# Performance work log

Measured on AMD Instinct MI355X. Metric: run time of the kernel, lower is better.

The kernel has to match this reference:

```python
import jax, jax.numpy as jnp
import numpy as np

N_HEADS = 64
N_KV_HEADS = 8
HEAD_DIM = 128
HIDDEN = 8192
SEQ = 2048


def setup_inputs() -> dict:
    key = jax.random.key(0)
    k1, k2, k3, k4 = jax.random.split(key, 4)
    scale = 1.0 / np.sqrt(HIDDEN)
    x = jax.random.normal(k1, (1, 1, SEQ, HIDDEN), dtype=jnp.float32)
    wq = jax.random.normal(k2, (HIDDEN, N_HEADS * HEAD_DIM), dtype=jnp.float32) * scale
    wk = jax.random.normal(k3, (HIDDEN, N_KV_HEADS * HEAD_DIM), dtype=jnp.float32) * scale
    wv = jax.random.normal(k4, (HIDDEN, N_KV_HEADS * HEAD_DIM), dtype=jnp.float32) * scale
    return {"x": x, "wq": wq, "wk": wk, "wv": wv}


def reference(x, wq, wk, wv):
    # Fused QKV projection: concat weights along output dim, single matmul.
    qkv_w = jnp.concatenate([wq, wk, wv], axis=-1)  # [H, (64+8+8)*128]
    fused = jnp.einsum('bush,hd->busd', x, qkv_w)    # [1,1,S,10240]
    b, _, s, _ = fused.shape
    q_dim = N_HEADS * HEAD_DIM
    kv_dim = N_KV_HEADS * HEAD_DIM
    q = fused[..., :q_dim]
    k = fused[..., q_dim:q_dim + kv_dim]
    v = fused[..., q_dim + kv_dim:]
    # nlp_create_qkv_heads: [B,1,S,nh*hd] -> [B,nh,S,hd]
    q_heads = q.reshape(b, s, N_HEADS, HEAD_DIM).transpose(0, 2, 1, 3)
    k_heads = k.reshape(b, s, N_KV_HEADS, HEAD_DIM).transpose(0, 2, 1, 3)
    v_heads = v.reshape(b, s, N_KV_HEADS, HEAD_DIM).transpose(0, 2, 1, 3)
    return (q_heads, k_heads, v_heads)
```

## Files before the change

### kernel.cpp

```cpp
#include <hip/hip_runtime.h>
#include <stdint.h>

#define M_DIM 2048
#define K_DIM 8192
#define N_Q   8192
#define N_KV  1024
#define BM    128
#define BN    128
#define BK    32
#define NIT   (K_DIM / BK)

typedef __bf16 bf16x8 __attribute__((ext_vector_type(8)));
typedef __bf16 bf16x2 __attribute__((ext_vector_type(2)));
typedef float  f32x4  __attribute__((ext_vector_type(4)));

__device__ __forceinline__ uint32_t swz(uint32_t r) { return ((r >> 1) ^ (r >> 3)) & 3u; }

__device__ __forceinline__ uint32_t pack_bf16(float lo, float hi) {
    bf16x2 v = { (__bf16)lo, (__bf16)hi };
    return __builtin_bit_cast(uint32_t, v);
}

__global__ __launch_bounds__(256) void qkv_gemm(
    const float* __restrict__ x,
    const float* __restrict__ wq,
    const float* __restrict__ wk,
    const float* __restrict__ wv,
    float* __restrict__ out)
{
    __shared__ __align__(16) uint16_t sA[BM * BK];
    __shared__ __align__(16) uint16_t sB[BN * BK];
    uint32_t* sAu = (uint32_t*)sA;
    uint32_t* sBu = (uint32_t*)sB;

    const uint32_t tid    = threadIdx.x;
    const uint32_t bid    = blockIdx.x;
    const uint32_t mt_blk = bid & 15;
    const uint32_t nt_blk = bid >> 4;
    const uint32_t m0     = mt_blk * BM;

    const size_t QSZ = (size_t)64 * M_DIM * 128;
    const size_t KSZ = (size_t)8  * M_DIM * 128;
    const float* Wsel;
    uint32_t ldW, col0;
    size_t obase;
    if (nt_blk < 64)      { Wsel = wq; ldW = N_Q;  col0 = nt_blk * 128;
                            obase = (size_t)nt_blk * M_DIM * 128; }
    else if (nt_blk < 72) { Wsel = wk; ldW = N_KV; col0 = (nt_blk - 64) * 128;
                            obase = QSZ + (size_t)(nt_blk - 64) * M_DIM * 128; }
    else                  { Wsel = wv; ldW = N_KV; col0 = (nt_blk - 72) * 128;
                            obase = QSZ + KSZ + (size_t)(nt_blk - 72) * M_DIM * 128; }

    const float* agp = x + (size_t)(m0 + (tid >> 3)) * K_DIM + (tid & 7) * 4;
    uint32_t a_wr[4];
    #pragma unroll
    for (int i = 0; i < 4; ++i) {
        uint32_t r = i * 32 + (tid >> 3);
        a_wr[i] = r * 16 + ((((tid >> 1) & 3) ^ swz(r)) * 4) + (tid & 1) * 2;
    }

    const uint32_t bk  = (tid >> 4) * 2;
    const uint32_t bn0 = (tid & 15) * 8;
    const float* bgp = Wsel + (size_t)bk * ldW + col0 + bn0;
    const uint32_t bkc = bk >> 3;
    const uint32_t bkd = (bk & 7) >> 1;

    f32x4 apre[4], bpre[4];
    #pragma unroll
    for (int i = 0; i < 4; ++i) apre[i] = *(const f32x4*)(agp + (size_t)i * 32 * K_DIM);
    bpre[0] = *(const f32x4*)(bgp);
    bpre[1] = *(const f32x4*)(bgp + 4);
    bpre[2] = *(const f32x4*)(bgp + ldW);
    bpre[3] = *(const f32x4*)(bgp + ldW + 4);

    const uint32_t lane = tid & 63;
    const uint32_t wid  = tid >> 6;
    const uint32_t wm   = (wid >> 1) * 64;
    const uint32_t wn   = (wid & 1) * 64;
    const uint32_t l15  = lane & 15;
    const uint32_t quad = lane >> 4;

    f32x4 acc[4][4] = {};

    uint32_t a_off[4], b_off[4];
    #pragma unroll
    for (int t = 0; t < 4; ++t) {
        uint32_t ar = wm + t * 16 + l15;
        a_off[t] = ar * BK + ((quad ^ swz(ar)) * 8);
        uint32_t br = wn + t * 16 + l15;
        b_off[t] = br * BK + ((quad ^ swz(br)) * 8);
    }

    const float* agp_n = agp + BK;
    const float* bgp_n = bgp + (size_t)BK * ldW;

    for (uint32_t kt = 0; kt < NIT; ++kt) {
        __syncthreads();

        #pragma unroll
        for (int i = 0; i < 4; ++i) {
            uint2 w;
            w.x = pack_bf16(apre[i].x, apre[i].y);
            w.y = pack_bf16(apre[i].z, apre[i].w);
            *(uint2*)&sAu[a_wr[i]] = w;
        }
        {
            const float* pk0 = (const float*)&bpre[0];
            const float* pk1 = (const float*)&bpre[2];
            #pragma unroll
            for (int j = 0; j < 8; ++j) {
                uint32_t n = bn0 + j;
                sBu[n * 16 + ((bkc ^ swz(n)) * 4) + bkd] = pack_bf16(pk0[j], pk1[j]);
            }
        }

        if (kt + 1 < NIT) {
            #pragma unroll
            for (int i = 0; i < 4; ++i) apre[i] = *(const f32x4*)(agp_n + (size_t)i * 32 * K_DIM);
            bpre[0] = *(const f32x4*)(bgp_n);
            bpre[1] = *(const f32x4*)(bgp_n + 4);
            bpre[2] = *(const f32x4*)(bgp_n + ldW);
            bpre[3] = *(const f32x4*)(bgp_n + ldW + 4);
            agp_n += BK;
            bgp_n += (size_t)BK * ldW;
        }

        __syncthreads();

        bf16x8 af[4], bf[4];
        #pragma unroll
        for (int t = 0; t < 4; ++t) {
            af[t] = *(const bf16x8*)(sA + a_off[t]);
            bf[t] = *(const bf16x8*)(sB + b_off[t]);
        }
        #pragma unroll
        for (int mt = 0; mt < 4; ++mt)
            #pragma unroll
            for (int nt = 0; nt < 4; ++nt)
                acc[mt][nt] = __builtin_amdgcn_mfma_f32_16x16x32_bf16(
                    af[mt], bf[nt], acc[mt][nt], 0, 0, 0);
    }

    float* op = out + obase + (size_t)m0 * 128;
    #pragma unroll
    for (int mt = 0; mt < 4; ++mt) {
        #pragma unroll
        for (int r = 0; r < 4; ++r) {
            uint32_t row = wm + mt * 16 + quad * 4 + r;
            #pragma unroll
            for (int nt = 0; nt < 4; ++nt) {
                uint32_t col = wn + nt * 16 + l15;
                op[(size_t)row * 128 + col] = acc[mt][nt][r];
            }
        }
    }
}

extern "C" void kernel_launch(void* const* d_in, const int* in_sizes, int n_in,
                              void* d_out, int out_size, void* d_ws, size_t ws_size,
                              hipStream_t stream) {
    const float* x  = (const float*)d_in[0];
    const float* wq = (const float*)d_in[1];
    const float* wk = (const float*)d_in[2];
    const float* wv = (const float*)d_in[3];
    qkv_gemm<<<dim3((M_DIM / BM) * ((N_Q + 2 * N_KV) / BN)), dim3(256), 0, stream>>>(
        x, wq, wk, wv, (float*)d_out);
}
```

Baseline: 1.032 ms.

## Pre-cast inputs to bf16 in workspace and use direct global-to-LDS GEMM

Adds separate kernels that convert x to bf16 and convert plus transpose the concatenated weights into a K-contiguous bf16 workspace. A new GEMM kernel then streams both operands with global_load_lds 16-byte loads straight into swizzled LDS, and remaps block order for cache locality. This removes per-iteration fp32 loads and in-register conversion and transposed scalar LDS stores. In exchange it pays extra memory passes over the inputs and has no double buffering. It falls back to the old kernel when workspace is too small.

```diff
diff --git a/kernel.cpp b/kernel.cpp
--- a/kernel.cpp
+++ b/kernel.cpp
@@ -5,6 +5,7 @@
 #define K_DIM 8192
 #define N_Q   8192
 #define N_KV  1024
+#define N_TOT (N_Q + 2 * N_KV)
 #define BM    128
 #define BN    128
 #define BK    32
@@ -14,7 +15,147 @@
 typedef __bf16 bf16x2 __attribute__((ext_vector_type(2)));
 typedef float  f32x4  __attribute__((ext_vector_type(4)));
 
-__device__ __forceinline__ uint32_t swz(uint32_t r) { return ((r >> 1) ^ (r >> 3)) & 3u; }
+__global__ __launch_bounds__(256) void xcast(const float* __restrict__ x,
+                                             __bf16* __restrict__ xb) {
+    size_t i = ((size_t)blockIdx.x * 256 + threadIdx.x) * 8;
+    f32x4 a = *(const f32x4*)(x + i);
+    f32x4 b = *(const f32x4*)(x + i + 4);
+    bf16x8 o = { (__bf16)a.x, (__bf16)a.y, (__bf16)a.z, (__bf16)a.w,
+                 (__bf16)b.x, (__bf16)b.y, (__bf16)b.z, (__bf16)b.w };
+    *(bf16x8*)(xb + i) = o;
+}
+
+__global__ __launch_bounds__(256) void wcast_t(const float* __restrict__ wq,
+                                               const float* __restrict__ wk,
+                                               const float* __restrict__ wv,
+                                               __bf16* __restrict__ wt) {
+    __shared__ float sT[64 * 65];
+    const uint32_t bid   = blockIdx.x;
+    const uint32_t ktile = bid & 127;
+    const uint32_t ntile = bid >> 7;
+    const float* W; uint32_t ldW, csrc, cdst;
+    if (ntile < 128)      { W = wq; ldW = N_Q;  csrc = ntile * 64;
+                            cdst = csrc; }
+    else if (ntile < 144) { W = wk; ldW = N_KV; csrc = (ntile - 128) * 64;
+                            cdst = N_Q + csrc; }
+    else                  { W = wv; ldW = N_KV; csrc = (ntile - 144) * 64;
+                            cdst = N_Q + N_KV + csrc; }
+    const uint32_t k0 = ktile * 64;
+    const uint32_t t  = threadIdx.x;
+
+    const uint32_t lr = t >> 4;
+    const uint32_t lc = (t & 15) * 4;
+    const float* gp = W + (size_t)(k0 + lr) * ldW + csrc + lc;
+    #pragma unroll
+    for (int i = 0; i < 4; ++i) {
+        f32x4 v = *(const f32x4*)(gp + (size_t)i * 16 * ldW);
+        float* d = &sT[(lr + i * 16) * 65 + lc];
+        d[0] = v.x; d[1] = v.y; d[2] = v.z; d[3] = v.w;
+    }
+    __syncthreads();
+
+    const uint32_t wn  = t >> 3;
+    const uint32_t wk8 = (t & 7) * 8;
+    #pragma unroll
+    for (int it = 0; it < 2; ++it) {
+        uint32_t n = wn + it * 32;
+        bf16x8 o;
+        #pragma unroll
+        for (int j = 0; j < 8; ++j) o[j] = (__bf16)sT[(wk8 + j) * 65 + n];
+        *(bf16x8*)(wt + (size_t)(cdst + n) * K_DIM + k0 + wk8) = o;
+    }
+}
+
+__device__ __forceinline__ void gload16(const void* g, void* l) {
+    __builtin_amdgcn_global_load_lds(
+        (const __attribute__((address_space(1))) void*)g,
+        (__attribute__((address_space(3))) void*)l, 16, 0, 0);
+}
+
+__global__ __launch_bounds__(256) void qkv_mm(const __bf16* __restrict__ xb,
+                                              const __bf16* __restrict__ wt,
+                                              float* __restrict__ out) {
+    __shared__ __align__(16) __bf16 sA[BM * BK];
+    __shared__ __align__(16) __bf16 sB[BN * BK];
+
+    const uint32_t tid = threadIdx.x;
+
+    const uint32_t logical = (blockIdx.x & 7) * 160 + (blockIdx.x >> 3);
+    const uint32_t mt = logical & 15;
+    const uint32_t nt = logical >> 4;
+    const uint32_t m0 = mt * BM;
+    const uint32_t n0 = nt * BN;
+
+    const uint32_t w    = tid >> 6;
+    const uint32_t lane = tid & 63;
+    const __bf16* gA[2];
+    const __bf16* gB[2];
+    #pragma unroll
+    for (int i = 0; i < 2; ++i) {
+        uint32_t c  = w * 128 + i * 64 + lane;
+        uint32_t r  = c >> 2;
+        uint32_t qs = (c & 3) ^ ((r >> 1) & 3);
+        gA[i] = xb + (size_t)(m0 + r) * K_DIM + qs * 8;
+        gB[i] = wt + (size_t)(n0 + r) * K_DIM + qs * 8;
+    }
+    char* la = (char*)sA + w * 2048;
+    char* lb = (char*)sB + w * 2048;
+
+    const uint32_t wm   = (w >> 1) * 64;
+    const uint32_t wn   = (w & 1) * 64;
+    const uint32_t l15  = lane & 15;
+    const uint32_t quad = lane >> 4;
+
+    uint32_t a_off[4], b_off[4];
+    #pragma unroll
+    for (int t = 0; t < 4; ++t) {
+        uint32_t ar = wm + t * 16 + l15;
+        a_off[t] = ar * BK + ((quad ^ ((ar >> 1) & 3)) * 8);
+        uint32_t br = wn + t * 16 + l15;
+        b_off[t] = br * BK + ((quad ^ ((br >> 1) & 3)) * 8);
+    }
+
+    f32x4 acc[4][4] = {};
+
+    for (uint32_t kt = 0; kt < NIT; ++kt) {
+        gload16(gA[0], la);        gload16(gA[1], la + 1024);
+        gload16(gB[0], lb);        gload16(gB[1], lb + 1024);
+        gA[0] += BK; gA[1] += BK; gB[0] += BK; gB[1] += BK;
+
+        __syncthreads();
+
+        bf16x8 af[4], bf[4];
+        #pragma unroll
+        for (int t = 0; t < 4; ++t) {
+            af[t] = *(const bf16x8*)(sA + a_off[t]);
+            bf[t] = *(const bf16x8*)(sB + b_off[t]);
+        }
+        #pragma unroll
+        for (int mi = 0; mi < 4; ++mi)
+            #pragma unroll
+            for (int ni = 0; ni < 4; ++ni)
+                acc[mi][ni] = __builtin_amdgcn_mfma_f32_16x16x32_bf16(
+                    af[mi], bf[ni], acc[mi][ni], 0, 0, 0);
+
+        __syncthreads();
+    }
+
+    float* op = out + (size_t)nt * (M_DIM * 128) + (size_t)m0 * 128;
+    #pragma unroll
+    for (int mi = 0; mi < 4; ++mi) {
+        #pragma unroll
+        for (int r = 0; r < 4; ++r) {
+            uint32_t row = wm + mi * 16 + quad * 4 + r;
+            #pragma unroll
+            for (int ni = 0; ni < 4; ++ni) {
+                uint32_t col = wn + ni * 16 + l15;
+                op[(size_t)row * 128 + col] = acc[mi][ni][r];
+            }
+        }
+    }
+}
+
+__device__ __forceinline__ uint32_t swz_fb(uint32_t r) { return ((r >> 1) ^ (r >> 3)) & 3u; }
 
 __device__ __forceinline__ uint32_t pack_bf16(float lo, float hi) {
     bf16x2 v = { (__bf16)lo, (__bf16)hi };
@@ -56,7 +197,7 @@
     #pragma unroll
     for (int i = 0; i < 4; ++i) {
         uint32_t r = i * 32 + (tid >> 3);
-        a_wr[i] = r * 16 + ((((tid >> 1) & 3) ^ swz(r)) * 4) + (tid & 1) * 2;
+        a_wr[i] = r * 16 + ((((tid >> 1) & 3) ^ swz_fb(r)) * 4) + (tid & 1) * 2;
     }
 
     const uint32_t bk  = (tid >> 4) * 2;
@@ -86,9 +227,9 @@
     #pragma unroll
     for (int t = 0; t < 4; ++t) {
         uint32_t ar = wm + t * 16 + l15;
-        a_off[t] = ar * BK + ((quad ^ swz(ar)) * 8);
+        a_off[t] = ar * BK + ((quad ^ swz_fb(ar)) * 8);
         uint32_t br = wn + t * 16 + l15;
-        b_off[t] = br * BK + ((quad ^ swz(br)) * 8);
+        b_off[t] = br * BK + ((quad ^ swz_fb(br)) * 8);
     }
 
     const float* agp_n = agp + BK;
@@ -99,10 +240,10 @@
 
         #pragma unroll
         for (int i = 0; i < 4; ++i) {
-            uint2 w;
-            w.x = pack_bf16(apre[i].x, apre[i].y);
-            w.y = pack_bf16(apre[i].z, apre[i].w);
-            *(uint2*)&sAu[a_wr[i]] = w;
+            uint2 wv2;
+            wv2.x = pack_bf16(apre[i].x, apre[i].y);
+            wv2.y = pack_bf16(apre[i].z, apre[i].w);
+            *(uint2*)&sAu[a_wr[i]] = wv2;
         }
         {
             const float* pk0 = (const float*)&bpre[0];
@@ -110,7 +251,7 @@
             #pragma unroll
             for (int j = 0; j < 8; ++j) {
                 uint32_t n = bn0 + j;
-                sBu[n * 16 + ((bkc ^ swz(n)) * 4) + bkd] = pack_bf16(pk0[j], pk1[j]);
+                sBu[n * 16 + ((bkc ^ swz_fb(n)) * 4) + bkd] = pack_bf16(pk0[j], pk1[j]);
             }
         }
 
@@ -134,23 +275,23 @@
             bf[t] = *(const bf16x8*)(sB + b_off[t]);
         }
         #pragma unroll
-        for (int mt = 0; mt < 4; ++mt)
-            #pragma unroll
-            for (int nt = 0; nt < 4; ++nt)
-                acc[mt][nt] = __builtin_amdgcn_mfma_f32_16x16x32_bf16(
-                    af[mt], bf[nt], acc[mt][nt], 0, 0, 0);
+        for (int mi = 0; mi < 4; ++mi)
+            #pragma unroll
+            for (int ni = 0; ni < 4; ++ni)
+                acc[mi][ni] = __builtin_amdgcn_mfma_f32_16x16x32_bf16(
+                    af[mi], bf[ni], acc[mi][ni], 0, 0, 0);
     }
 
     float* op = out + obase + (size_t)m0 * 128;
     #pragma unroll
-    for (int mt = 0; mt < 4; ++mt) {
+    for (int mi = 0; mi < 4; ++mi) {
         #pragma unroll
         for (int r = 0; r < 4; ++r) {
-            uint32_t row = wm + mt * 16 + quad * 4 + r;
-            #pragma unroll
-            for (int nt = 0; nt < 4; ++nt) {
-                uint32_t col = wn + nt * 16 + l15;
-                op[(size_t)row * 128 + col] = acc[mt][nt][r];
+            uint32_t row = wm + mi * 16 + quad * 4 + r;
+            #pragma unroll
+            for (int ni = 0; ni < 4; ++ni) {
+                uint32_t col = wn + ni * 16 + l15;
+                op[(size_t)row * 128 + col] = acc[mi][ni][r];
             }
         }
     }
@@ -163,6 +304,18 @@
     const float* wq = (const float*)d_in[1];
     const float* wk = (const float*)d_in[2];
     const float* wv = (const float*)d_in[3];
-    qkv_gemm<<<dim3((M_DIM / BM) * ((N_Q + 2 * N_KV) / BN)), dim3(256), 0, stream>>>(
-        x, wq, wk, wv, (float*)d_out);
-}
+
+    const size_t XB_BYTES = (size_t)M_DIM * K_DIM * 2;
+    const size_t WT_BYTES = (size_t)N_TOT * K_DIM * 2;
+
+    if (ws_size >= XB_BYTES + WT_BYTES) {
+        __bf16* xb = (__bf16*)d_ws;
+        __bf16* wt = (__bf16*)((char*)d_ws + XB_BYTES);
+        xcast<<<dim3((M_DIM * K_DIM) / (256 * 8)), dim3(256), 0, stream>>>(x, xb);
+        wcast_t<<<dim3((K_DIM / 64) * (N_TOT / 64)), dim3(256), 0, stream>>>(wq, wk, wv, wt);
+        qkv_mm<<<dim3((M_DIM / BM) * (N_TOT / BN)), dim3(256), 0, stream>>>(xb, wt, (float*)d_out);
+    } else {
+        qkv_gemm<<<dim3((M_DIM / BM) * (N_TOT / BN)), dim3(256), 0, stream>>>(
+            x, wq, wk, wv, (float*)d_out);
+    }
+}
```

Result: slower. 1.120 ms (+8.5%).
